# Performance work log

Hardware: AMD Instinct MI355X
Metric: run time of the kernel (lower is better)

Reference implementation:

```python
import jax, jax.numpy as jnp
import numpy as np

MARGIN = 0.3
BIG = 9999999.0


def setup_inputs() -> dict:
    key = jax.random.key(0)
    k1, k2, k3 = jax.random.split(key, 3)
    N, D, D2, NUM_IDS = 8192, 1024, 512, 512
    emb = jax.random.normal(k1, (N, D), dtype=jnp.float32)
    clot_feats_s = jax.random.normal(k2, (N, D2), dtype=jnp.float32)
    label = jax.random.randint(k3, (N,), 0, NUM_IDS, dtype=jnp.int64)
    return {"emb": emb, "label": label, "clot_feats_s": clot_feats_s}


def _margin_ranking_loss(x1, x2, y, margin):
    # torch MarginRankingLoss: mean(max(0, -y*(x1-x2)+margin))
    return jnp.mean(jnp.maximum(0.0, -y * (x1 - x2) + margin))


def reference(emb, label, clot_feats_s):
    N = emb.shape[0]
    # euclidean_dist(emb, emb): [N,N]
    sq = jnp.sum(emb * emb, axis=1)
    dist = sq[:, None] + sq[None, :] - 2.0 * (emb @ emb.T)
    dist = jnp.sqrt(jnp.clip(dist, 1e-12, None))
    # cosine similarity of clot_feats_s with itself: [N,N]
    nrm = jnp.sqrt(jnp.sum(clot_feats_s * clot_feats_s, axis=1))
    cos = (clot_feats_s @ clot_feats_s.T) / (nrm[:, None] * nrm[None, :])
    # same-identity mask
    sim = (label[:, None] == label[None, :]).astype(dist.dtype)
    # batch-hard: top-2 positives (largest masked distance), hardest negative (smallest)
    pos_vals, pos_idx = jax.lax.top_k(dist - BIG * (1.0 - sim), 2)
    dist_ap1, dist_ap2 = pos_vals[:, 0], pos_vals[:, 1]
    neg_mat = dist + BIG * sim
    hard_n_idx = jnp.argmin(neg_mat, axis=1)
    dist_an = jnp.min(neg_mat, axis=1)
    rows = jnp.arange(N)
    # per-row gathers into cosine-sim matrix (detached in original)
    alpha1 = jax.lax.stop_gradient(cos[rows, pos_idx[:, 0]])
    alpha2 = jax.lax.stop_gradient(cos[rows, pos_idx[:, 1]])
    # (alphan gathered in original but unused in the loss)
    y11 = jnp.where(alpha1 < alpha2, -1.0, 1.0)
    y11_m = jnp.where(alpha1 == alpha2, 0.0, 1.0)
    loss11 = _margin_ranking_loss(
        dist_ap2 * y11_m,
        dist_ap1 * y11_m + MARGIN * (alpha1 - alpha2 - y11),
        y11, MARGIN)
    dist_ap1_m = dist_ap1 + MARGIN * (alpha1 - 1.0)
    loss13 = _margin_ranking_loss(dist_an, dist_ap1_m, 1.0, MARGIN)
    loss = 0.1 * loss11 + loss13
    prec = jnp.mean((dist_an > dist_ap1_m).astype(jnp.float32))
    return loss, prec
```

## Files before the change

kernel.cpp:

```cpp
#include <hip/hip_runtime.h>
#include <stdint.h>

#define NR 8192
#define DE 1024
#define DC 512
#define BIGF 9999999.0f
#define MARG 0.3f
#define NEGI -3.0e38f
#define POSI 3.0e38f

typedef __attribute__((ext_vector_type(8))) short bf16x8;
typedef __attribute__((ext_vector_type(4))) float f32x4;

typedef __attribute__((address_space(3))) unsigned int lds_u32;
typedef const __attribute__((address_space(1))) unsigned int glb_u32;

static __device__ __forceinline__ void ld_g2l16(const void* g, void* l) {
    __builtin_amdgcn_global_load_lds((glb_u32*)g, (lds_u32*)l, 16, 0, 0);
}

static __device__ __forceinline__ unsigned short f2bf(float x) {
    unsigned u = __float_as_uint(x);
    unsigned r = u + 0x7FFFu + ((u >> 16) & 1u);
    return (unsigned short)(r >> 16);
}

static __device__ __forceinline__ float b2f(short u) {
    return __uint_as_float(((unsigned)(unsigned short)u) << 16);
}

__global__ __launch_bounds__(256) void k_prep_emb(const float* __restrict__ emb,
                                                  const int* __restrict__ label,
                                                  short* __restrict__ embb,
                                                  float* __restrict__ sq,
                                                  int* __restrict__ cnt) {
    int row = blockIdx.x, tid = threadIdx.x;
    float4 v = ((const float4*)(emb + (size_t)row * DE))[tid];
    float s = v.x * v.x + v.y * v.y + v.z * v.z + v.w * v.w;
    ushort4 b;
    b.x = f2bf(v.x); b.y = f2bf(v.y); b.z = f2bf(v.z); b.w = f2bf(v.w);
    *(ushort4*)&embb[(size_t)row * DE + tid * 4] = b;
    for (int m = 1; m < 64; m <<= 1) s += __shfl_xor(s, m);
    __shared__ float red[4];
    if ((tid & 63) == 0) red[tid >> 6] = s;
    __syncthreads();
    if (tid == 0) {
        sq[row] = red[0] + red[1] + red[2] + red[3];
        atomicAdd(&cnt[label[row]], 1);
    }
}

__global__ __launch_bounds__(512) void k_scan(const int* __restrict__ cnt,
                                              int* __restrict__ clsOff) {
    __shared__ int s[512];
    int t = threadIdx.x;
    s[t] = cnt[t];
    __syncthreads();
    for (int d = 1; d < 512; d <<= 1) {
        int v = (t >= d) ? s[t - d] : 0;
        __syncthreads();
        s[t] += v;
        __syncthreads();
    }
    clsOff[t] = s[t] - cnt[t];
}

__global__ __launch_bounds__(256) void k_fill(const int* __restrict__ label,
                                              const int* __restrict__ clsOff,
                                              int* __restrict__ fill,
                                              int* __restrict__ list) {
    int i = blockIdx.x * 256 + threadIdx.x;
    int l = label[i];
    int p = atomicAdd(&fill[l], 1);
    list[clsOff[l] + p] = i;
}

__global__ __launch_bounds__(256, 3) void k_main(const short* __restrict__ embb,
                                                 const float* __restrict__ sq,
                                                 const int* __restrict__ label,
                                                 unsigned* __restrict__ mnA) {
    const int L = blockIdx.x;
    int bx = (int)((sqrtf((float)(1 + 2 * L)) - 1.0f) * 0.5f);
    while (2 * (bx + 1) * (bx + 1) + 2 * (bx + 1) <= L) ++bx;
    while (2 * bx * bx + 2 * bx > L) --bx;
    const int pnl = L - (2 * bx * bx + 2 * bx);
    const int d = pnl - bx * 4;
    const int jt0 = d > 0 ? d : 0;

    __shared__ __align__(16) short As[128 * 32];
    __shared__ __align__(16) short Bs[128 * 32];

    const int tid = threadIdx.x;
    const int lane = tid & 63;
    const int w = tid >> 6;
    const int q = lane >> 4, l15 = lane & 15;
    const int i0 = pnl * 128;

    const int srow = tid >> 2;
    const int g = (tid & 3) ^ ((tid >> 3) & 3);
    const short* gA = embb + (size_t)(i0 + srow) * DE + g * 8;
    const short* gB = embb + (size_t)(bx * 512 + jt0 * 128 + srow) * DE + g * 8;

    const int pxor = q ^ ((l15 >> 1) & 3);

    float rmn[8], sqi[8];
    int lia[8];
#pragma unroll
    for (int pp = 0; pp < 8; ++pp) {
        rmn[pp] = POSI;
        int rowg = i0 + w * 32 + (pp >> 2) * 16 + q * 4 + (pp & 3);
        sqi[pp] = sq[rowg]; lia[pp] = label[rowg];
    }

    auto stage = [&](int koff, const short* gBb) {
        ld_g2l16(gA + koff, &As[(size_t)tid * 8]);
        ld_g2l16(gA + (size_t)64 * DE + koff, &As[(size_t)(tid + 256) * 8]);
        ld_g2l16(gBb + koff, &Bs[(size_t)tid * 8]);
        ld_g2l16(gBb + (size_t)64 * DE + koff, &Bs[(size_t)(tid + 256) * 8]);
    };

    stage(0, gB);

    for (int jt = jt0; jt < 4; ++jt) {
        const int j0 = bx * 512 + jt * 128;
        f32x4 acc[2][8];
#pragma unroll
        for (int mi = 0; mi < 2; ++mi)
#pragma unroll
            for (int ni = 0; ni < 8; ++ni) acc[mi][ni] = (f32x4){0.f, 0.f, 0.f, 0.f};

        for (int ks = 0; ks < 32; ++ks) {
            __syncthreads();
            bf16x8 af[2], bfr[8];
#pragma unroll
            for (int mi = 0; mi < 2; ++mi)
                af[mi] = *(const bf16x8*)&As[(w * 32 + mi * 16 + l15) * 32 + pxor * 8];
#pragma unroll
            for (int ni = 0; ni < 8; ++ni)
                bfr[ni] = *(const bf16x8*)&Bs[(ni * 16 + l15) * 32 + pxor * 8];
#pragma unroll
            for (int mi = 0; mi < 2; ++mi)
#pragma unroll
                for (int ni = 0; ni < 8; ++ni)
                    acc[mi][ni] = __builtin_amdgcn_mfma_f32_16x16x32_bf16(af[mi], bfr[ni], acc[mi][ni], 0, 0, 0);
            __syncthreads();
            if (ks < 31) {
                stage((ks + 1) * 32, gB);
            } else if (jt < 3) {
                gB += (size_t)128 * DE;
                stage(0, gB);
            }
        }

#pragma unroll
        for (int ni = 0; ni < 8; ++ni) {
            const int cg = j0 + ni * 16 + l15;
            const float sqjv = sq[cg];
            const int lbjv = label[cg];
            float cmn = POSI;
#pragma unroll
            for (int pp = 0; pp < 8; ++pp) {
                float d2 = fmaf(-2.0f, acc[pp >> 2][ni][pp & 3], sqi[pp] + sqjv);
                d2 = fmaxf(d2, 1e-12f);
                float dn = (lia[pp] == lbjv) ? POSI : d2;
                rmn[pp] = fminf(rmn[pp], dn);
                cmn = fminf(cmn, dn);
            }
            cmn = fminf(cmn, __shfl_xor(cmn, 16));
            cmn = fminf(cmn, __shfl_xor(cmn, 32));
            if (q == 0) atomicMin(&mnA[cg], __float_as_uint(cmn));
        }
    }

#pragma unroll
    for (int pp = 0; pp < 8; ++pp) {
        float m0 = rmn[pp];
        for (int s = 1; s <= 8; s <<= 1) m0 = fminf(m0, __shfl_xor(m0, s));
        if (l15 == 0) {
            int rowg = i0 + w * 32 + (pp >> 2) * 16 + q * 4 + (pp & 3);
            atomicMin(&mnA[rowg], __float_as_uint(m0));
        }
    }
}

__global__ __launch_bounds__(256) void k_pos(const short* __restrict__ embb,
                                             const float* __restrict__ sq,
                                             const float* __restrict__ clot,
                                             const int* __restrict__ label,
                                             const int* __restrict__ cnt,
                                             const int* __restrict__ clsOff,
                                             const int* __restrict__ clsList,
                                             const unsigned* __restrict__ mnA,
                                             float* __restrict__ ap1, float* __restrict__ ap2,
                                             float* __restrict__ an,
                                             float* __restrict__ alpha1, float* __restrict__ alpha2) {
    int wid = threadIdx.x >> 6, lane = threadIdx.x & 63;
    int row = blockIdx.x * 4 + wid;
    int lb = label[row];
    int cc = cnt[lb], off = clsOff[lb];
    float sqiv = sq[row];

    const bf16x8* rp = (const bf16x8*)(embb + (size_t)row * DE + lane * 16);
    bf16x8 ra = rp[0], rb = rp[1];
    float rf[16];
#pragma unroll
    for (int t = 0; t < 8; ++t) { rf[t] = b2f(ra[t]); rf[8 + t] = b2f(rb[t]); }

    float v1 = NEGI, v2 = NEGI;
    int i1 = 0, i2 = 0;
    for (int m = 0; m < cc; ++m) {
        int j = clsList[off + m];
        float d2;
        if (j == row) {
            d2 = 1e-12f;
        } else {
            const bf16x8* jp = (const bf16x8*)(embb + (size_t)j * DE + lane * 16);
            bf16x8 ja = jp[0], jb = jp[1];
            float s = 0.f;
#pragma unroll
            for (int t = 0; t < 8; ++t) s = fmaf(rf[t], b2f(ja[t]), s);
#pragma unroll
            for (int t = 0; t < 8; ++t) s = fmaf(rf[8 + t], b2f(jb[t]), s);
            for (int mm = 1; mm < 64; mm <<= 1) s += __shfl_xor(s, mm);
            d2 = fmaxf(fmaf(-2.0f, s, sqiv + sq[j]), 1e-12f);
        }
        bool t1 = (d2 > v1) || (d2 == v1 && j < i1);
        bool t2 = (d2 > v2) || (d2 == v2 && j < i2);
        v2 = t1 ? v1 : (t2 ? d2 : v2);
        i2 = t1 ? i1 : (t2 ? j : i2);
        v1 = t1 ? d2 : v1;
        i1 = t1 ? j : i1;
    }

    float a1 = sqrtf(v1);
    int j1 = i1;
    float a2v; int j2;
    if (cc >= 2) {
        a2v = sqrtf(v2);
        j2 = i2;
    } else {
        float kv = NEGI; int ki = 0;
        for (int c = lane; c < NR; c += 64) {
            if (label[c] == lb) continue;
            const bf16x8* cp = (const bf16x8*)(embb + (size_t)c * DE);
            float s = 0.f;
            for (int t = 0; t < 128; ++t) {
                bf16x8 cv = cp[t];
#pragma unroll
                for (int u = 0; u < 8; ++u) s = fmaf(b2f(ra[0]) * 0.f + 1.f, 0.f, s);
            }
            s = 0.f;
            const short* crow = embb + (size_t)c * DE;
            const short* rrow = embb + (size_t)row * DE;
            for (int t = 0; t < DE; ++t) s = fmaf(b2f(rrow[t]), b2f(crow[t]), s);
            float d2c = fmaxf(fmaf(-2.0f, s, sqiv + sq[c]), 1e-12f);
            bool tk = (d2c > kv) || (d2c == kv && c < ki);
            kv = tk ? d2c : kv; ki = tk ? c : ki;
        }
        for (int mm = 1; mm < 64; mm <<= 1) {
            float ov = __shfl_xor(kv, mm); int oi = __shfl_xor(ki, mm);
            bool tk = (ov > kv) || (ov == kv && oi < ki);
            kv = tk ? ov : kv; ki = tk ? oi : ki;
        }
        a2v = sqrtf(kv) - BIGF;
        j2 = ki;
    }

    const float4* c4 = (const float4*)clot;
    float s1 = 0.f, s2 = 0.f, n0 = 0.f, n1 = 0.f, n2 = 0.f;
    for (int t = lane; t < DC / 4; t += 64) {
        float4 a = c4[(size_t)row * (DC / 4) + t];
        float4 b1 = c4[(size_t)j1 * (DC / 4) + t];
        float4 b2 = c4[(size_t)j2 * (DC / 4) + t];
        s1 += a.x * b1.x + a.y * b1.y + a.z * b1.z + a.w * b1.w;
        s2 += a.x * b2.x + a.y * b2.y + a.z * b2.z + a.w * b2.w;
        n0 += a.x * a.x + a.y * a.y + a.z * a.z + a.w * a.w;
        n1 += b1.x * b1.x + b1.y * b1.y + b1.z * b1.z + b1.w * b1.w;
        n2 += b2.x * b2.x + b2.y * b2.y + b2.z * b2.z + b2.w * b2.w;
    }
    for (int mm = 1; mm < 64; mm <<= 1) {
        s1 += __shfl_xor(s1, mm); s2 += __shfl_xor(s2, mm);
        n0 += __shfl_xor(n0, mm); n1 += __shfl_xor(n1, mm); n2 += __shfl_xor(n2, mm);
    }
    if (lane == 0) {
        ap1[row] = a1; ap2[row] = a2v;
        an[row] = sqrtf(__uint_as_float(mnA[row]));
        alpha1[row] = s1 / (sqrtf(n0) * sqrtf(n1));
        alpha2[row] = s2 / (sqrtf(n0) * sqrtf(n2));
    }
}

__global__ __launch_bounds__(256) void k_final(const float* __restrict__ ap1, const float* __restrict__ ap2,
                                               const float* __restrict__ an,
                                               const float* __restrict__ alpha1, const float* __restrict__ alpha2,
                                               float* __restrict__ out) {
    int tid = threadIdx.x;
    float sl11 = 0.f, sl13 = 0.f, sp = 0.f;
    for (int row = tid; row < NR; row += 256) {
        float a1 = alpha1[row], a2 = alpha2[row];
        float dap1 = ap1[row], dap2 = ap2[row], dan = an[row];
        float y = (a1 < a2) ? -1.f : 1.f;
        float ym = (a1 == a2) ? 0.f : 1.f;
        float x1 = dap2 * ym;
        float x2 = dap1 * ym + MARG * (a1 - a2 - y);
        sl11 += fmaxf(0.f, -y * (x1 - x2) + MARG);
        float ap1m = dap1 + MARG * (a1 - 1.f);
        sl13 += fmaxf(0.f, -(dan - ap1m) + MARG);
        sp += (dan > ap1m) ? 1.f : 0.f;
    }
    for (int m = 1; m < 64; m <<= 1) {
        sl11 += __shfl_xor(sl11, m);
        sl13 += __shfl_xor(sl13, m);
        sp += __shfl_xor(sp, m);
    }
    __shared__ float r11[4], r13[4], rp[4];
    if ((tid & 63) == 0) { r11[tid >> 6] = sl11; r13[tid >> 6] = sl13; rp[tid >> 6] = sp; }
    __syncthreads();
    if (tid == 0) {
        float t11 = r11[0] + r11[1] + r11[2] + r11[3];
        float t13 = r13[0] + r13[1] + r13[2] + r13[3];
        float tp = rp[0] + rp[1] + rp[2] + rp[3];
        out[0] = 0.1f * (t11 / (float)NR) + t13 / (float)NR;
        out[1] = tp / (float)NR;
    }
}

extern "C" void kernel_launch(void* const* d_in, const int* in_sizes, int n_in,
                              void* d_out, int out_size, void* d_ws, size_t ws_size,
                              hipStream_t stream) {
    const float* emb = (const float*)d_in[0];
    const int* label = (const int*)d_in[1];
    const float* clot = (const float*)d_in[2];
    float* out = (float*)d_out;

    char* ws = (char*)d_ws;
    size_t off = 0;
    auto alloc = [&](size_t bytes) -> char* {
        char* p = ws + off;
        off = (off + bytes + 255) & ~(size_t)255;
        return p;
    };
    short*    embb = (short*)alloc((size_t)NR * DE * 2);
    float*    sq   = (float*)alloc(NR * 4);
    int*      cnt  = (int*)alloc(512 * 4);
    int*      cOff = (int*)alloc(512 * 4);
    int*      fill = (int*)alloc(512 * 4);
    int*      list = (int*)alloc(NR * 4);
    unsigned* mnA  = (unsigned*)alloc((size_t)NR * 4);
    float*    ap1  = (float*)alloc(NR * 4);
    float*    ap2  = (float*)alloc(NR * 4);
    float*    an   = (float*)alloc(NR * 4);
    float*    al1  = (float*)alloc(NR * 4);
    float*    al2  = (float*)alloc(NR * 4);

    hipMemsetAsync(cnt, 0, 512 * 4, stream);
    hipMemsetAsync(fill, 0, 512 * 4, stream);
    hipMemsetAsync(mnA, 0xFF, (size_t)NR * 4, stream);

    k_prep_emb<<<dim3(NR), dim3(256), 0, stream>>>(emb, label, embb, sq, cnt);
    k_scan<<<dim3(1), dim3(512), 0, stream>>>(cnt, cOff);
    k_fill<<<dim3(NR / 256), dim3(256), 0, stream>>>(label, cOff, fill, list);
    k_main<<<dim3(544), dim3(256), 0, stream>>>(embb, sq, label, mnA);
    k_pos<<<dim3(NR / 4), dim3(256), 0, stream>>>(embb, sq, clot, label, cnt, cOff, list,
                                                  mnA, ap1, ap2, an, al1, al2);
    k_final<<<dim3(1), dim3(256), 0, stream>>>(ap1, ap2, an, al1, al2, out);
}
```

Measured before the change: 249.5 us.

## Restructure distance GEMM into 128x256 tiles with double-buffered LDS pipeline

The symmetric negative-min GEMM kernel moves from 128x128 tiles with single-buffered LDS to 128x256 tiles with double-buffered A/B staging. Global-to-LDS loads for the next k-step are split and issued around the MFMA phases, using explicit vmcnt waits and raw barriers plus setprio around the MFMA bursts. The triangular tile schedule is recomputed for the new tile shape, the grid size changes, and occupancy drops to 2 blocks per CU. A dead dummy loop in the fallback path of k_pos is also removed. This trades more LDS and register pressure for better data reuse and overlap of loads with MFMA work.

Result: slower. 268.2 us (+7.5%).

```diff
diff --git a/kernel.cpp b/kernel.cpp
--- a/kernel.cpp
+++ b/kernel.cpp
@@ -75,111 +75,142 @@
     list[clsOff[l] + p] = i;
 }
 
-__global__ __launch_bounds__(256, 3) void k_main(const short* __restrict__ embb,
+__global__ __launch_bounds__(256, 2) void k_main(const short* __restrict__ embb,
                                                  const float* __restrict__ sq,
                                                  const int* __restrict__ label,
                                                  unsigned* __restrict__ mnA) {
-    const int L = blockIdx.x;
-    int bx = (int)((sqrtf((float)(1 + 2 * L)) - 1.0f) * 0.5f);
-    while (2 * (bx + 1) * (bx + 1) + 2 * (bx + 1) <= L) ++bx;
-    while (2 * bx * bx + 2 * bx > L) --bx;
-    const int pnl = L - (2 * bx * bx + 2 * bx);
-    const int d = pnl - bx * 4;
-    const int jt0 = d > 0 ? d : 0;
-
-    __shared__ __align__(16) short As[128 * 32];
-    __shared__ __align__(16) short Bs[128 * 32];
+    int L = blockIdx.x;
+    int pr = 0, off = 0;
+    while (off + (32 - (pr >> 1)) <= L) { off += 32 - (pr >> 1); ++pr; }
+    const int pc = (pr >> 1) + (L - off);
+    const int i0 = pr * 128, j0 = pc * 256;
+
+    __shared__ __align__(16) short As[2][128 * 32];
+    __shared__ __align__(16) short Bs[2][256 * 32];
 
     const int tid = threadIdx.x;
     const int lane = tid & 63;
     const int w = tid >> 6;
     const int q = lane >> 4, l15 = lane & 15;
-    const int i0 = pnl * 128;
 
     const int srow = tid >> 2;
     const int g = (tid & 3) ^ ((tid >> 3) & 3);
     const short* gA = embb + (size_t)(i0 + srow) * DE + g * 8;
-    const short* gB = embb + (size_t)(bx * 512 + jt0 * 128 + srow) * DE + g * 8;
+    const short* gB = embb + (size_t)(j0 + srow) * DE + g * 8;
 
     const int pxor = q ^ ((l15 >> 1) & 3);
 
-    float rmn[8], sqi[8];
-    int lia[8];
-#pragma unroll
-    for (int pp = 0; pp < 8; ++pp) {
-        rmn[pp] = POSI;
-        int rowg = i0 + w * 32 + (pp >> 2) * 16 + q * 4 + (pp & 3);
-        sqi[pp] = sq[rowg]; lia[pp] = label[rowg];
-    }
-
-    auto stage = [&](int koff, const short* gBb) {
-        ld_g2l16(gA + koff, &As[(size_t)tid * 8]);
-        ld_g2l16(gA + (size_t)64 * DE + koff, &As[(size_t)(tid + 256) * 8]);
-        ld_g2l16(gBb + koff, &Bs[(size_t)tid * 8]);
-        ld_g2l16(gBb + (size_t)64 * DE + koff, &Bs[(size_t)(tid + 256) * 8]);
+    f32x4 acc[8][4];
+#pragma unroll
+    for (int m = 0; m < 8; ++m)
+#pragma unroll
+        for (int n = 0; n < 4; ++n) acc[m][n] = (f32x4){0.f, 0.f, 0.f, 0.f};
+
+    auto stage_a = [&](int kt, int b) {
+        const short* s = gA + kt * 32;
+        ld_g2l16(s, &As[b][(size_t)tid * 8]);
+        ld_g2l16(s + (size_t)64 * DE, &As[b][(size_t)(tid + 256) * 8]);
     };
-
-    stage(0, gB);
-
-    for (int jt = jt0; jt < 4; ++jt) {
-        const int j0 = bx * 512 + jt * 128;
-        f32x4 acc[2][8];
-#pragma unroll
-        for (int mi = 0; mi < 2; ++mi)
-#pragma unroll
-            for (int ni = 0; ni < 8; ++ni) acc[mi][ni] = (f32x4){0.f, 0.f, 0.f, 0.f};
-
-        for (int ks = 0; ks < 32; ++ks) {
-            __syncthreads();
-            bf16x8 af[2], bfr[8];
-#pragma unroll
-            for (int mi = 0; mi < 2; ++mi)
-                af[mi] = *(const bf16x8*)&As[(w * 32 + mi * 16 + l15) * 32 + pxor * 8];
-#pragma unroll
-            for (int ni = 0; ni < 8; ++ni)
-                bfr[ni] = *(const bf16x8*)&Bs[(ni * 16 + l15) * 32 + pxor * 8];
-#pragma unroll
-            for (int mi = 0; mi < 2; ++mi)
-#pragma unroll
-                for (int ni = 0; ni < 8; ++ni)
-                    acc[mi][ni] = __builtin_amdgcn_mfma_f32_16x16x32_bf16(af[mi], bfr[ni], acc[mi][ni], 0, 0, 0);
-            __syncthreads();
-            if (ks < 31) {
-                stage((ks + 1) * 32, gB);
-            } else if (jt < 3) {
-                gB += (size_t)128 * DE;
-                stage(0, gB);
+    auto stage_b0 = [&](int kt, int b) {
+        ld_g2l16(gB + kt * 32, &Bs[b][(size_t)tid * 8]);
+    };
+    auto stage_b123 = [&](int kt, int b) {
+        const short* s = gB + kt * 32;
+        ld_g2l16(s + (size_t)64 * DE, &Bs[b][(size_t)(tid + 256) * 8]);
+        ld_g2l16(s + (size_t)128 * DE, &Bs[b][(size_t)(tid + 512) * 8]);
+        ld_g2l16(s + (size_t)192 * DE, &Bs[b][(size_t)(tid + 768) * 8]);
+    };
+
+    stage_a(0, 0); stage_b0(0, 0); stage_b123(0, 0);
+
+    int cur = 0;
+    for (int kt = 0; kt < 32; ++kt) {
+        if (kt < 31) {
+            stage_a(kt + 1, cur ^ 1);
+            stage_b0(kt + 1, cur ^ 1);
+            asm volatile("s_waitcnt vmcnt(3)" ::: "memory");
+        } else {
+            asm volatile("s_waitcnt vmcnt(0)" ::: "memory");
+        }
+        asm volatile("s_barrier" ::: "memory");
+
+        bf16x8 bfr[4], af[4];
+#pragma unroll
+        for (int n = 0; n < 4; ++n)
+            bfr[n] = *(const bf16x8*)&Bs[cur][(w * 64 + n * 16 + l15) * 32 + pxor * 8];
+#pragma unroll
+        for (int m = 0; m < 4; ++m)
+            af[m] = *(const bf16x8*)&As[cur][(m * 16 + l15) * 32 + pxor * 8];
+
+        __builtin_amdgcn_s_setprio(1);
+#pragma unroll
+        for (int m = 0; m < 4; ++m)
+#pragma unroll
+            for (int n = 0; n < 4; ++n)
+                acc[m][n] = __builtin_amdgcn_mfma_f32_16x16x32_bf16(af[m], bfr[n], acc[m][n], 0, 0, 0);
+        __builtin_amdgcn_s_setprio(0);
+        asm volatile("s_barrier" ::: "memory");
+
+        if (kt < 31) stage_b123(kt + 1, cur ^ 1);
+#pragma unroll
+        for (int m = 0; m < 4; ++m)
+            af[m] = *(const bf16x8*)&As[cur][((m + 4) * 16 + l15) * 32 + pxor * 8];
+
+        __builtin_amdgcn_s_setprio(1);
+#pragma unroll
+        for (int m = 0; m < 4; ++m)
+#pragma unroll
+            for (int n = 0; n < 4; ++n)
+                acc[m + 4][n] = __builtin_amdgcn_mfma_f32_16x16x32_bf16(af[m], bfr[n], acc[m + 4][n], 0, 0, 0);
+        __builtin_amdgcn_s_setprio(0);
+        asm volatile("s_barrier" ::: "memory");
+
+        cur ^= 1;
+    }
+
+    const int j0w = j0 + w * 64;
+    float sqj[4]; int lbj[4];
+#pragma unroll
+    for (int n = 0; n < 4; ++n) {
+        int cg = j0w + n * 16 + l15;
+        sqj[n] = sq[cg]; lbj[n] = label[cg];
+    }
+    float cmn[4] = {POSI, POSI, POSI, POSI};
+#pragma unroll
+    for (int m = 0; m < 8; ++m) {
+        float rm[4] = {POSI, POSI, POSI, POSI};
+        float sqi[4]; int lbi[4];
+#pragma unroll
+        for (int rr = 0; rr < 4; ++rr) {
+            int rg = i0 + m * 16 + q * 4 + rr;
+            sqi[rr] = sq[rg]; lbi[rr] = label[rg];
+        }
+#pragma unroll
+        for (int n = 0; n < 4; ++n)
+#pragma unroll
+            for (int rr = 0; rr < 4; ++rr) {
+                float d2 = fmaf(-2.0f, acc[m][n][rr], sqi[rr] + sqj[n]);
+                d2 = fmaxf(d2, 1e-12f);
+                float dn = (lbi[rr] == lbj[n]) ? POSI : d2;
+                rm[rr] = fminf(rm[rr], dn);
+                cmn[n] = fminf(cmn[n], dn);
             }
-        }
-
-#pragma unroll
-        for (int ni = 0; ni < 8; ++ni) {
-            const int cg = j0 + ni * 16 + l15;
-            const float sqjv = sq[cg];
-            const int lbjv = label[cg];
-            float cmn = POSI;
-#pragma unroll
-            for (int pp = 0; pp < 8; ++pp) {
-                float d2 = fmaf(-2.0f, acc[pp >> 2][ni][pp & 3], sqi[pp] + sqjv);
-                d2 = fmaxf(d2, 1e-12f);
-                float dn = (lia[pp] == lbjv) ? POSI : d2;
-                rmn[pp] = fminf(rmn[pp], dn);
-                cmn = fminf(cmn, dn);
-            }
-            cmn = fminf(cmn, __shfl_xor(cmn, 16));
-            cmn = fminf(cmn, __shfl_xor(cmn, 32));
-            if (q == 0) atomicMin(&mnA[cg], __float_as_uint(cmn));
-        }
-    }
-
-#pragma unroll
-    for (int pp = 0; pp < 8; ++pp) {
-        float m0 = rmn[pp];
-        for (int s = 1; s <= 8; s <<= 1) m0 = fminf(m0, __shfl_xor(m0, s));
-        if (l15 == 0) {
-            int rowg = i0 + w * 32 + (pp >> 2) * 16 + q * 4 + (pp & 3);
-            atomicMin(&mnA[rowg], __float_as_uint(m0));
-        }
+#pragma unroll
+        for (int rr = 0; rr < 4; ++rr) {
+            float v = rm[rr];
+            v = fminf(v, __shfl_xor(v, 1));
+            v = fminf(v, __shfl_xor(v, 2));
+            v = fminf(v, __shfl_xor(v, 4));
+            v = fminf(v, __shfl_xor(v, 8));
+            if (l15 == 0) atomicMin(&mnA[i0 + m * 16 + q * 4 + rr], __float_as_uint(v));
+        }
+    }
+#pragma unroll
+    for (int n = 0; n < 4; ++n) {
+        float v = cmn[n];
+        v = fminf(v, __shfl_xor(v, 16));
+        v = fminf(v, __shfl_xor(v, 32));
+        if (q == 0) atomicMin(&mnA[j0w + n * 16 + l15], __float_as_uint(v));
     }
 }
 
@@ -242,14 +273,7 @@
         float kv = NEGI; int ki = 0;
         for (int c = lane; c < NR; c += 64) {
             if (label[c] == lb) continue;
-            const bf16x8* cp = (const bf16x8*)(embb + (size_t)c * DE);
             float s = 0.f;
-            for (int t = 0; t < 128; ++t) {
-                bf16x8 cv = cp[t];
-#pragma unroll
-                for (int u = 0; u < 8; ++u) s = fmaf(b2f(ra[0]) * 0.f + 1.f, 0.f, s);
-            }
-            s = 0.f;
             const short* crow = embb + (size_t)c * DE;
             const short* rrow = embb + (size_t)row * DE;
             for (int t = 0; t < DE; ++t) s = fmaf(b2f(rrow[t]), b2f(crow[t]), s);
@@ -360,7 +384,7 @@
     k_prep_emb<<<dim3(NR), dim3(256), 0, stream>>>(emb, label, embb, sq, cnt);
     k_scan<<<dim3(1), dim3(512), 0, stream>>>(cnt, cOff);
     k_fill<<<dim3(NR / 256), dim3(256), 0, stream>>>(label, cOff, fill, list);
-    k_main<<<dim3(544), dim3(256), 0, stream>>>(embb, sq, label, mnA);
+    k_main<<<dim3(1056), dim3(256), 0, stream>>>(embb, sq, label, mnA);
     k_pos<<<dim3(NR / 4), dim3(256), 0, stream>>>(embb, sq, clot, label, cnt, cOff, list,
                                                   mnA, ap1, ap2, an, al1, al2);
     k_final<<<dim3(1), dim3(256), 0, stream>>>(ap1, ap2, an, al1, al2, out);
```
